# Performance work log

Measured on AMD Instinct MI355X. Metric: run time of the kernel, lower is better.

Reference implementation:

```python
import jax, jax.numpy as jnp
import numpy as np

N = 50000   # total nodes across batched graphs
E = 800000  # total edges
F = 30      # input node features
G = 256     # number of graphs in the disjoint batch
CH = [128, 64, 32]
N_LABELS = 2


def setup_inputs() -> dict:
    key = jax.random.key(0)
    ks = jax.random.split(key, 16)
    x = jax.random.normal(ks[0], (N, F), dtype=jnp.float32)
    edge_weight = jax.random.uniform(ks[1], (E,), dtype=jnp.float32)
    edge_row = jax.random.randint(ks[2], (E,), 0, N, dtype=jnp.int32)
    edge_col = jax.random.randint(ks[3], (E,), 0, N, dtype=jnp.int32)
    seg = jnp.sort(jax.random.randint(ks[4], (N,), 0, G, dtype=jnp.int32))
    # GCSConv params: out = A @ (x W1) + x W2 + b, per layer
    dims = [F] + CH
    params = {}
    kk = 5
    for l in range(3):
        fin, fout = dims[l], dims[l + 1]
        s = 1.0 / np.sqrt(fin)
        params[f"w1_{l+1}"] = jax.random.uniform(ks[kk], (fin, fout), minval=-s, maxval=s, dtype=jnp.float32); kk += 1
        params[f"w2_{l+1}"] = jax.random.uniform(ks[kk], (fin, fout), minval=-s, maxval=s, dtype=jnp.float32); kk += 1
        params[f"b_{l+1}"] = jnp.zeros((fout,), dtype=jnp.float32)
    sd = 1.0 / np.sqrt(CH[-1])
    params["wd"] = jax.random.uniform(ks[kk], (CH[-1], N_LABELS), minval=-sd, maxval=sd, dtype=jnp.float32)
    params["bd"] = jnp.zeros((N_LABELS,), dtype=jnp.float32)
    return {"x": x, "edge_weight": edge_weight, "edge_row": edge_row,
            "edge_col": edge_col, "seg": seg, **params}


def _gcs_conv(x, ew, er, ec, w1, w2, b):
    # spektral GCSConv: relu(A @ (x W1) + x W2 + b) with sparse A in COO form
    h = x @ w1                                   # [N, Fout]
    msgs = ew[:, None] * h[ec]                   # gather along edges [E, Fout]
    agg = jax.ops.segment_sum(msgs, er, num_segments=N)  # SpMM scatter [N, Fout]
    return jax.nn.relu(agg + x @ w2 + b)


def reference(x, edge_weight, edge_row, edge_col, seg,
              w1_1, w2_1, b_1, w1_2, w2_2, b_2, w1_3, w2_3, b_3, wd, bd):
    h = _gcs_conv(x, edge_weight, edge_row, edge_col, w1_1, w2_1, b_1)
    h = _gcs_conv(h, edge_weight, edge_row, edge_col, w1_2, w2_2, b_2)
    h = _gcs_conv(h, edge_weight, edge_row, edge_col, w1_3, w2_3, b_3)
    # GlobalAvgPool: segment mean over graph ids
    sums = jax.ops.segment_sum(h, seg, num_segments=G)               # [G, 32]
    cnts = jax.ops.segment_sum(jnp.ones((N,), h.dtype), seg, num_segments=G)
    pooled = sums / jnp.maximum(cnts, 1.0)[:, None]
    return jax.nn.softmax(pooled @ wd + bd, axis=-1)                 # [G, 2]
```

## Files before the change

kernel.cpp:

```cpp
#include <hip/hip_runtime.h>
#include <hip/hip_fp16.h>

#define N_NODES 50000
#define N_EDGES 800000
#define N_GRAPHS 256
#define NCB 196
#define CHUNK 3125
#define MBLK 782

typedef _Float16 f16x8 __attribute__((ext_vector_type(8)));
typedef float    f32x4 __attribute__((ext_vector_type(4)));

__global__ __launch_bounds__(256)
void hist_prep(const int* __restrict__ ER, const float* __restrict__ X,
               const int* __restrict__ SEG,
               const float* __restrict__ W1, const float* __restrict__ W2,
               const float* __restrict__ W12, const float* __restrict__ W22,
               const float* __restrict__ W13, const float* __restrict__ W23,
               int* __restrict__ ghist, __half* __restrict__ XPh,
               int* __restrict__ start,
               __half* __restrict__ W1f, __half* __restrict__ W2f,
               __half* __restrict__ W3f)
{
    int b = blockIdx.x;
    int t = threadIdx.x;
    if (b < 256) {
        __shared__ int h[NCB];
        for (int i = t; i < NCB; i += 256) h[i] = 0;
        __syncthreads();
        int lo = b * CHUNK, hi = lo + CHUNK;
        for (int e = lo + t; e < hi; e += 256) atomicAdd(&h[ER[e] >> 8], 1);
        __syncthreads();
        for (int i = t; i < NCB; i += 256) ghist[i * 256 + b] = h[i];
        return;
    }
    int bid = b - 256;
    if (bid < 782) {
        int idx = bid * 256 + t;
        int n = idx >> 2;
        int c4 = idx & 3;
        if (n >= N_NODES) return;
        __half2 hb[4];
        #pragma unroll
        for (int k = 0; k < 4; ++k) {
            int c0 = c4 * 8 + 2 * k;
            float v0 = (c0 < 30) ? X[n * 30 + c0] : 0.f;
            float v1 = (c0 + 1 < 30) ? X[n * 30 + c0 + 1] : 0.f;
            hb[k] = __float22half2_rn(make_float2(v0, v1));
        }
        *(uint4*)(XPh + (size_t)n * 32 + c4 * 8) = *(uint4*)&hb[0];
    } else if (bid < 978) {
        int n = (bid - 782) * 256 + t;
        if (n >= N_NODES) return;
        int g = SEG[n];
        int gprev = (n == 0) ? -1 : SEG[n - 1];
        for (int gg = gprev + 1; gg <= g; ++gg) start[gg] = n;
        if (n == N_NODES - 1)
            for (int gg = g + 1; gg <= N_GRAPHS; ++gg) start[gg] = N_NODES;
    } else {
        int idx = (bid - 978) * 256 + t;
        if (idx < 8192) {
            int i = idx & 7, c = (idx >> 3) & 15, g = (idx >> 7) & 3;
            int s = (idx >> 9) & 1, n = idx >> 10;
            int k = s * 32 + g * 8 + i, col = n * 16 + c;
            float w = 0.f;
            if (k < 30) w = W1[k * 128 + col];
            else if (k >= 32 && k < 62) w = W2[(k - 32) * 128 + col];
            W1f[idx] = __float2half(w);
        } else if (idx < 24576) {
            int o = idx - 8192;
            int i = o & 7, c = (o >> 3) & 15, g = (o >> 7) & 3;
            int s = (o >> 9) & 3, n = o >> 11;
            int k = s * 32 + g * 8 + i, col = n * 16 + c;
            float w = (col < 64) ? W12[k * 64 + col] : W22[k * 64 + col - 64];
            W2f[o] = __float2half(w);
        } else {
            int o = idx - 24576;
            int i = o & 7, c = (o >> 3) & 15, g = (o >> 7) & 3;
            int s = (o >> 9) & 1, n = o >> 10;
            int k = s * 32 + g * 8 + i, col = n * 16 + c;
            float w = (col < 32) ? W13[k * 32 + col] : W23[k * 32 + col - 32];
            W3f[o] = __float2half(w);
        }
    }
}

__global__ __launch_bounds__(256)
void scan1(int* __restrict__ ghist, int* __restrict__ bsum)
{
    __shared__ int s[256];
    int t = threadIdx.x, b = blockIdx.x;
    int i = b * 256 + t;
    int v = ghist[i];
    s[t] = v;
    __syncthreads();
    for (int off = 1; off < 256; off <<= 1) {
        int u = (t >= off) ? s[t - off] : 0;
        __syncthreads();
        s[t] += u;
        __syncthreads();
    }
    ghist[i] = s[t] - v;
    if (t == 255) bsum[b] = s[255];
}

__global__ __launch_bounds__(256)
void c_scatter(const int* __restrict__ ER, const int* __restrict__ EC,
               const float* __restrict__ EW, const int* __restrict__ ghist,
               const int* __restrict__ bsum, uint2* __restrict__ tmp)
{
    __shared__ int s[256];
    __shared__ int cur[NCB];
    int t = threadIdx.x, blk = blockIdx.x;
    int v = (t < NCB) ? bsum[t] : 0;
    s[t] = v;
    __syncthreads();
    for (int off = 1; off < 256; off <<= 1) {
        int u = (t >= off) ? s[t - off] : 0;
        __syncthreads();
        s[t] += u;
        __syncthreads();
    }
    if (t < NCB) cur[t] = (s[t] - v) + ghist[t * 256 + blk];
    __syncthreads();
    int lo = blk * CHUNK, hi = lo + CHUNK;
    for (int e = lo + t; e < hi; e += 256) {
        int d = ER[e];
        int pos = atomicAdd(&cur[d >> 8], 1);
        tmp[pos] = make_uint2((unsigned int)EC[e] | ((unsigned int)(d & 255) << 16),
                              (unsigned int)__half_as_ushort(__float2half(EW[e])));
    }
}

__device__ __forceinline__ void fma8h(float4& a0, float4& a1, float w,
                                      const uint4& raw)
{
    const __half2* hp = (const __half2*)&raw;
    float2 f0 = __half22float2(hp[0]);
    float2 f1 = __half22float2(hp[1]);
    float2 f2 = __half22float2(hp[2]);
    float2 f3 = __half22float2(hp[3]);
    a0.x = fmaf(w, f0.x, a0.x); a0.y = fmaf(w, f0.y, a0.y);
    a0.z = fmaf(w, f1.x, a0.z); a0.w = fmaf(w, f1.y, a0.w);
    a1.x = fmaf(w, f2.x, a1.x); a1.y = fmaf(w, f2.y, a1.y);
    a1.z = fmaf(w, f3.x, a1.z); a1.w = fmaf(w, f3.y, a1.w);
}

__device__ __forceinline__ unsigned int relu2(unsigned int u)
{
    unsigned int lo = (u & 0x8000u)     ? 0u : (u & 0x0000FFFFu);
    unsigned int hi = (u & 0x80000000u) ? 0u : (u & 0xFFFF0000u);
    return lo | hi;
}

__global__ __launch_bounds__(1024)
void bsort(const uint2* __restrict__ tmp, const int* __restrict__ bsum,
           unsigned int* __restrict__ packed, int* __restrict__ rowptr)
{
    __shared__ int s[256];
    __shared__ int hist[256];
    __shared__ int cur[256];
    int t = threadIdx.x, b = blockIdx.x;

    if (t < 256) s[t] = (t < NCB) ? bsum[t] : 0;
    __syncthreads();
    for (int off = 1; off < 256; off <<= 1) {
        int u = 0;
        if (t < 256 && t >= off) u = s[t - off];
        __syncthreads();
        if (t < 256) s[t] += u;
        __syncthreads();
    }
    int cntb = bsum[b];
    int base = s[b] - cntb;
    int end  = base + cntb;
    __syncthreads();

    if (t < 256) hist[t] = 0;
    __syncthreads();
    for (int j = base + t; j < end; j += 1024)
        atomicAdd(&hist[(tmp[j].x >> 16) & 255], 1);
    __syncthreads();
    int hv = 0;
    if (t < 256) { hv = hist[t]; s[t] = hv; }
    __syncthreads();
    for (int off = 1; off < 256; off <<= 1) {
        int u = 0;
        if (t < 256 && t >= off) u = s[t - off];
        __syncthreads();
        if (t < 256) s[t] += u;
        __syncthreads();
    }
    if (t < 256) {
        int excl = s[t] - hv;
        int n = b * 256 + t;
        if (n < N_NODES) rowptr[n] = base + excl;
        if (b == NCB - 1 && t == 0) rowptr[N_NODES] = N_EDGES;
        cur[t] = base + excl;
    }
    __syncthreads();
    for (int j = base + t; j < end; j += 1024) {
        uint2 v = tmp[j];
        int pos = atomicAdd(&cur[(v.x >> 16) & 255], 1);
        packed[pos] = (v.x & 0xFFFF) | (v.y << 16);
    }
}

__global__ __launch_bounds__(512)
void dense12_mfma(const __half* __restrict__ XPh, const int* __restrict__ rowptr,
                  const unsigned int* __restrict__ packed,
                  const __half* __restrict__ W1f, const float* __restrict__ B1,
                  const __half* __restrict__ W2f, const float* __restrict__ B2,
                  __half* __restrict__ H2h, __half* __restrict__ A2h)
{
    __shared__ __align__(16) __half As[64 * 72];
    __shared__ __align__(16) __half Hs[64 * 136];
    const int tid = threadIdx.x;
    const int m0 = blockIdx.x * 64;

    if (tid < 256) {
        int row = tid >> 2, c4 = tid & 3;
        int gm = m0 + row;
        uint4 v = make_uint4(0, 0, 0, 0);
        if (gm < N_NODES) v = *(const uint4*)(XPh + (size_t)gm * 32 + c4 * 8);
        *(uint4*)(As + row * 72 + (4 + c4) * 8) = v;
    }
    {
        int local = tid >> 3;
        int es = (tid >> 2) & 1;
        int q = tid & 3;
        int n = m0 + local;
        float4 acc0 = make_float4(0.f, 0.f, 0.f, 0.f);
        float4 acc1 = make_float4(0.f, 0.f, 0.f, 0.f);
        if (n < N_NODES) {
            int r0 = rowptr[n], r1 = rowptr[n + 1];
            int mid = (r0 + r1) >> 1;
            int lo = es ? mid : r0;
            int hi = es ? r1 : mid;
            int j = lo;
            for (; j + 3 < hi; j += 4) {
                unsigned int ra = packed[j],     rb = packed[j + 1];
                unsigned int rc = packed[j + 2], rd = packed[j + 3];
                uint4 rawa = *(const uint4*)(XPh + (size_t)(ra & 0xFFFF) * 32 + q * 8);
                uint4 rawb = *(const uint4*)(XPh + (size_t)(rb & 0xFFFF) * 32 + q * 8);
                uint4 rawc = *(const uint4*)(XPh + (size_t)(rc & 0xFFFF) * 32 + q * 8);
                uint4 rawd = *(const uint4*)(XPh + (size_t)(rd & 0xFFFF) * 32 + q * 8);
                float wa = __half2float(__ushort_as_half((unsigned short)(ra >> 16)));
                float wb = __half2float(__ushort_as_half((unsigned short)(rb >> 16)));
                float wc = __half2float(__ushort_as_half((unsigned short)(rc >> 16)));
                float wd = __half2float(__ushort_as_half((unsigned short)(rd >> 16)));
                fma8h(acc0, acc1, wa, rawa);
                fma8h(acc0, acc1, wb, rawb);
                fma8h(acc0, acc1, wc, rawc);
                fma8h(acc0, acc1, wd, rawd);
            }
            for (; j < hi; ++j) {
                unsigned int r = packed[j];
                uint4 raw = *(const uint4*)(XPh + (size_t)(r & 0xFFFF) * 32 + q * 8);
                float wv = __half2float(__ushort_as_half((unsigned short)(r >> 16)));
                fma8h(acc0, acc1, wv, raw);
            }
        }
        float* part = (float*)Hs;
        if (es == 1) {
            *(float4*)&part[local * 36 + q * 8 + 0] = acc0;
            *(float4*)&part[local * 36 + q * 8 + 4] = acc1;
        }
        __syncthreads();
        if (es == 0) {
            float4 p0 = *(float4*)&part[local * 36 + q * 8 + 0];
            float4 p1 = *(float4*)&part[local * 36 + q * 8 + 4];
            acc0.x += p0.x; acc0.y += p0.y; acc0.z += p0.z; acc0.w += p0.w;
            acc1.x += p1.x; acc1.y += p1.y; acc1.z += p1.z; acc1.w += p1.w;
            __half2 hb2[4];
            hb2[0] = __float22half2_rn(make_float2(acc0.x, acc0.y));
            hb2[1] = __float22half2_rn(make_float2(acc0.z, acc0.w));
            hb2[2] = __float22half2_rn(make_float2(acc1.x, acc1.y));
            hb2[3] = __float22half2_rn(make_float2(acc1.z, acc1.w));
            *(uint4*)(As + local * 72 + q * 8) = *(uint4*)&hb2[0];
        }
    }
    __syncthreads();

    const int lane = tid & 63;
    const int w  = tid >> 6;
    const int lr = lane & 15;
    const int lg = lane >> 4;

    f32x4 acc[4];
    #pragma unroll
    for (int m = 0; m < 4; ++m) acc[m] = (f32x4){0.f, 0.f, 0.f, 0.f};

    #pragma unroll
    for (int s = 0; s < 2; ++s) {
        f16x8 b = *(const f16x8*)(W1f + (((w * 2 + s) * 4 + lg) * 16 + lr) * 8);
        #pragma unroll
        for (int m = 0; m < 4; ++m) {
            f16x8 a = *(const f16x8*)(As + (m * 16 + lr) * 72 + s * 32 + lg * 8);
            acc[m] = __builtin_amdgcn_mfma_f32_16x16x32_f16(a, b, acc[m], 0, 0, 0);
        }
    }

    {
        const float bias = B1[w * 16 + lr];
        #pragma unroll
        for (int m = 0; m < 4; ++m)
            #pragma unroll
            for (int r = 0; r < 4; ++r) {
                float v = fmaxf(acc[m][r] + bias, 0.f);
                Hs[(m * 16 + lg * 4 + r) * 136 + w * 16 + lr] = __float2half(v);
            }
    }
    __syncthreads();

    f32x4 acc2[4];
    #pragma unroll
    for (int m = 0; m < 4; ++m) acc2[m] = (f32x4){0.f, 0.f, 0.f, 0.f};

    #pragma unroll
    for (int s = 0; s < 4; ++s) {
        f16x8 b = *(const f16x8*)(W2f + (((w * 4 + s) * 4 + lg) * 16 + lr) * 8);
        #pragma unroll
        for (int m = 0; m < 4; ++m) {
            f16x8 a = *(const f16x8*)(Hs + (m * 16 + lr) * 136 + s * 32 + lg * 8);
            acc2[m] = __builtin_amdgcn_mfma_f32_16x16x32_f16(a, b, acc2[m], 0, 0, 0);
        }
    }
    __syncthreads();

    {
        const float bias = (w >= 4) ? B2[(w - 4) * 16 + lr] : 0.f;
        #pragma unroll
        for (int m = 0; m < 4; ++m)
            #pragma unroll
            for (int r = 0; r < 4; ++r)
                Hs[(m * 16 + lg * 4 + r) * 136 + w * 16 + lr] =
                    __float2half(acc2[m][r] + bias);
    }
    __syncthreads();

    for (int idx = tid; idx < 1024; idx += 512) {
        int row = idx >> 4, c8 = idx & 15;
        int gm = m0 + row;
        if (gm < N_NODES) {
            uint4 v = *(const uint4*)(Hs + row * 136 + c8 * 8);
            if (c8 < 8) *(uint4*)(H2h + (size_t)gm * 64 + c8 * 8) = v;
            else        *(uint4*)(A2h + (size_t)gm * 64 + (c8 - 8) * 8) = v;
        }
    }
}

__global__ __launch_bounds__(256)
void dense3_mfma(const __half* __restrict__ X, const __half* __restrict__ W3f,
                 const float* __restrict__ B3, __half* __restrict__ H3h,
                 __half* __restrict__ B2h)
{
    __shared__ __align__(16) __half As[64 * 72];
    __shared__ __align__(16) __half Os[64 * 72];
    const int tid = threadIdx.x;
    const int m0 = blockIdx.x * 64;
    const int lane = tid & 63;
    const int w  = tid >> 6;
    const int lr = lane & 15;
    const int lg = lane >> 4;

    for (int idx = tid; idx < 512; idx += 256) {
        int row = idx >> 3, c8 = idx & 7;
        int gm = m0 + row;
        uint4 v = make_uint4(0, 0, 0, 0);
        if (gm < N_NODES) v = *(const uint4*)(X + (size_t)gm * 64 + c8 * 8);
        v.x = relu2(v.x); v.y = relu2(v.y); v.z = relu2(v.z); v.w = relu2(v.w);
        *(uint4*)(As + row * 72 + c8 * 8) = v;
    }
    __syncthreads();

    f32x4 acc[4];
    #pragma unroll
    for (int m = 0; m < 4; ++m) acc[m] = (f32x4){0.f, 0.f, 0.f, 0.f};

    #pragma unroll
    for (int s = 0; s < 2; ++s) {
        f16x8 b = *(const f16x8*)(W3f + (((w * 2 + s) * 4 + lg) * 16 + lr) * 8);
        #pragma unroll
        for (int m = 0; m < 4; ++m) {
            f16x8 a = *(const f16x8*)(As + (m * 16 + lr) * 72 + s * 32 + lg * 8);
            acc[m] = __builtin_amdgcn_mfma_f32_16x16x32_f16(a, b, acc[m], 0, 0, 0);
        }
    }

    const float bias = (w >= 2) ? B3[(w - 2) * 16 + lr] : 0.f;
    #pragma unroll
    for (int m = 0; m < 4; ++m)
        #pragma unroll
        for (int r = 0; r < 4; ++r)
            Os[(m * 16 + lg * 4 + r) * 72 + w * 16 + lr] =
                __float2half(acc[m][r] + bias);
    __syncthreads();

    for (int idx = tid; idx < 512; idx += 256) {
        int row = idx >> 3, c8 = idx & 7;
        int gm = m0 + row;
        if (gm < N_NODES) {
            uint4 v = *(const uint4*)(Os + row * 72 + c8 * 8);
            if (c8 < 4) *(uint4*)(H3h + (size_t)gm * 32 + c8 * 8) = v;
            else        *(uint4*)(B2h + (size_t)gm * 32 + (c8 - 4) * 8) = v;
        }
    }
}

template<int FOUT, int S>
__global__ __launch_bounds__(512)
void spmm_split(const __half* __restrict__ H, const int* __restrict__ rowptr,
                const unsigned int* __restrict__ packed, __half* __restrict__ AGGh)
{
    constexpr int T = FOUT / 8;
    constexpr int NPB = 512 / (S * T);
    __shared__ float part[NPB][S - 1][FOUT + 4];
    int tid = threadIdx.x;
    int local = tid / (S * T);
    int rem = tid % (S * T);
    int s = rem / T;
    int q = rem % T;
    int n = blockIdx.x * NPB + local;
    bool valid = (n < N_NODES);
    float4 acc0 = make_float4(0.f, 0.f, 0.f, 0.f);
    float4 acc1 = make_float4(0.f, 0.f, 0.f, 0.f);
    __half* ap = AGGh + (size_t)n * FOUT + q * 8;
    if (valid) {
        int r0 = rowptr[n], r1 = rowptr[n + 1];
        int deg = r1 - r0;
        int lo = r0 + (deg * s) / S;
        int hi = r0 + (deg * (s + 1)) / S;
        if (s == 0) {
            uint4 raw = *(const uint4*)ap;
            const __half2* hp = (const __half2*)&raw;
            float2 f0 = __half22float2(hp[0]);
            float2 f1 = __half22float2(hp[1]);
            float2 f2 = __half22float2(hp[2]);
            float2 f3 = __half22float2(hp[3]);
            acc0 = make_float4(f0.x, f0.y, f1.x, f1.y);
            acc1 = make_float4(f2.x, f2.y, f3.x, f3.y);
        }
        int j = lo;
        for (; j + 3 < hi; j += 4) {
            unsigned int ra = packed[j],     rb = packed[j + 1];
            unsigned int rc = packed[j + 2], rd = packed[j + 3];
            uint4 rawa = *(const uint4*)(H + (size_t)(ra & 0xFFFF) * FOUT + q * 8);
            uint4 rawb = *(const uint4*)(H + (size_t)(rb & 0xFFFF) * FOUT + q * 8);
            uint4 rawc = *(const uint4*)(H + (size_t)(rc & 0xFFFF) * FOUT + q * 8);
            uint4 rawd = *(const uint4*)(H + (size_t)(rd & 0xFFFF) * FOUT + q * 8);
            float wa = __half2float(__ushort_as_half((unsigned short)(ra >> 16)));
            float wb = __half2float(__ushort_as_half((unsigned short)(rb >> 16)));
            float wc = __half2float(__ushort_as_half((unsigned short)(rc >> 16)));
            float wd = __half2float(__ushort_as_half((unsigned short)(rd >> 16)));
            fma8h(acc0, acc1, wa, rawa);
            fma8h(acc0, acc1, wb, rawb);
            fma8h(acc0, acc1, wc, rawc);
            fma8h(acc0, acc1, wd, rawd);
        }
        for (; j < hi; ++j) {
            unsigned int r = packed[j];
            uint4 raw = *(const uint4*)(H + (size_t)(r & 0xFFFF) * FOUT + q * 8);
            float w = __half2float(__ushort_as_half((unsigned short)(r >> 16)));
            fma8h(acc0, acc1, w, raw);
        }
    }
    if (s > 0) {
        *(float4*)&part[local][s - 1][q * 8 + 0] = acc0;
        *(float4*)&part[local][s - 1][q * 8 + 4] = acc1;
    }
    __syncthreads();
    if (s == 0 && valid) {
        #pragma unroll
        for (int ss = 0; ss < S - 1; ++ss) {
            float4 p0 = *(float4*)&part[local][ss][q * 8 + 0];
            float4 p1 = *(float4*)&part[local][ss][q * 8 + 4];
            acc0.x += p0.x; acc0.y += p0.y; acc0.z += p0.z; acc0.w += p0.w;
            acc1.x += p1.x; acc1.y += p1.y; acc1.z += p1.z; acc1.w += p1.w;
        }
        __half2 hb[4];
        hb[0] = __float22half2_rn(make_float2(acc0.x, acc0.y));
        hb[1] = __float22half2_rn(make_float2(acc0.z, acc0.w));
        hb[2] = __float22half2_rn(make_float2(acc1.x, acc1.y));
        hb[3] = __float22half2_rn(make_float2(acc1.z, acc1.w));
        *(uint4*)ap = *(uint4*)&hb[0];
    }
}

__global__ __launch_bounds__(1024)
void pool_kernel(const __half* __restrict__ H, const int* __restrict__ start,
                 const float* __restrict__ WD, const float* __restrict__ BD,
                 float* __restrict__ OUT)
{
    __shared__ float red[32][33];
    int g = blockIdx.x;
    int s = start[g], e = start[g + 1];
    int q = threadIdx.x & 31;
    int grp = threadIdx.x >> 5;
    float acc = 0.f;
    for (int n = s + grp; n < e; n += 32)
        acc += fmaxf(__half2float(H[(size_t)n * 32 + q]), 0.f);
    red[grp][q] = acc;
    __syncthreads();
    if (threadIdx.x < 32) {
        float v = 0.f;
        #pragma unroll
        for (int i = 0; i < 32; ++i) v += red[i][q];
        float inv = (e > s) ? 1.0f / (float)(e - s) : 1.0f;
        float p = v * inv;
        float p0 = p * WD[q * 2 + 0];
        float p1 = p * WD[q * 2 + 1];
        #pragma unroll
        for (int off = 16; off; off >>= 1) {
            p0 += __shfl_down(p0, off, 32);
            p1 += __shfl_down(p1, off, 32);
        }
        if (q == 0) {
            float l0 = p0 + BD[0], l1 = p1 + BD[1];
            float m = fmaxf(l0, l1);
            float e0 = expf(l0 - m), e1 = expf(l1 - m);
            float si = 1.0f / (e0 + e1);
            OUT[g * 2 + 0] = e0 * si;
            OUT[g * 2 + 1] = e1 * si;
        }
    }
}

extern "C" void kernel_launch(void* const* d_in, const int* in_sizes, int n_in,
                              void* d_out, int out_size, void* d_ws, size_t ws_size,
                              hipStream_t stream)
{
    const float* x    = (const float*)d_in[0];
    const float* ew   = (const float*)d_in[1];
    const int*   er   = (const int*)d_in[2];
    const int*   ec   = (const int*)d_in[3];
    const int*   seg  = (const int*)d_in[4];
    const float* w1_1 = (const float*)d_in[5];
    const float* w2_1 = (const float*)d_in[6];
    const float* b_1  = (const float*)d_in[7];
    const float* w1_2 = (const float*)d_in[8];
    const float* w2_2 = (const float*)d_in[9];
    const float* b_2  = (const float*)d_in[10];
    const float* w1_3 = (const float*)d_in[11];
    const float* w2_3 = (const float*)d_in[12];
    const float* b_3  = (const float*)d_in[13];
    const float* wd   = (const float*)d_in[14];
    const float* bd   = (const float*)d_in[15];

    float* ws = (float*)d_ws;
    int*   IW = (int*)d_ws;
    __half* XPh    = (__half*)ws;
    uint2*  tmp    = (uint2*)(ws + 1600000);
    __half* H2h    = (__half*)(ws + 3200000);
    __half* A2h    = (__half*)(ws + 4800000);
    __half* H3h    = (__half*)(ws + 6400000);
    __half* B2h    = (__half*)(ws + 7200000);
    unsigned int* packed = (unsigned int*)(IW + 8000000);
    int*    rowptr = IW + 9000000;
    int*    ghist  = IW + 9060000;
    int*    bsum   = IW + 9115000;
    int*    start  = IW + 9120000;
    __half* W1f    = (__half*)(ws + 9125000);
    __half* W2f    = (__half*)(ws + 9130000);
    __half* W3f    = (__half*)(ws + 9139000);

    dim3 blk(256);

    hist_prep<<<dim3(256 + 782 + 196 + 112), blk, 0, stream>>>(
        er, x, seg, w1_1, w2_1, w1_2, w2_2, w1_3, w2_3,
        ghist, XPh, start, W1f, W2f, W3f);
    scan1<<<dim3(NCB), blk, 0, stream>>>(ghist, bsum);
    c_scatter<<<dim3(256), blk, 0, stream>>>(er, ec, ew, ghist, bsum, tmp);
    bsort<<<dim3(NCB), dim3(1024), 0, stream>>>(tmp, bsum, packed, rowptr);

    dense12_mfma<<<dim3(MBLK), dim3(512), 0, stream>>>(XPh, rowptr, packed,
                                                       W1f, b_1, W2f, b_2,
                                                       H2h, A2h);
    spmm_split<64, 4><<<dim3((N_NODES + 15) / 16), dim3(512), 0, stream>>>(H2h, rowptr,
                                                                           packed, A2h);
    dense3_mfma<<<dim3(MBLK), blk, 0, stream>>>(A2h, W3f, b_3, H3h, B2h);
    spmm_split<32, 4><<<dim3((N_NODES + 31) / 32), dim3(512), 0, stream>>>(H3h, rowptr,
                                                                           packed, B2h);

    pool_kernel<<<dim3(N_GRAPHS), dim3(1024), 0, stream>>>(B2h, start, wd, bd,
                                                           (float*)d_out);
}
```

Before: 172.8 us.

## Fuse layer-2 SpMM aggregation with layer-3 dense MFMA into one kernel

Replaces the separate spmm_split<64,4> launch and dense3_mfma launch with a single 1024-thread kernel. Each block first aggregates the neighbour rows for its 64 nodes into shared memory, splitting each node's edges across two thread groups, then adds the self term, applies ReLU and runs the 16x16x32 MFMA for layer 3. This removes one launch and the global round trip of the layer-2 aggregate. In exchange, each block has only two edge splits per node instead of four, and the MFMA work is spread so each wave handles a single tile.

```diff
diff --git a/kernel.cpp b/kernel.cpp
--- a/kernel.cpp
+++ b/kernel.cpp
@@ -144,13 +144,6 @@
     a0.z = fmaf(w, f1.x, a0.z); a0.w = fmaf(w, f1.y, a0.w);
     a1.x = fmaf(w, f2.x, a1.x); a1.y = fmaf(w, f2.y, a1.y);
     a1.z = fmaf(w, f3.x, a1.z); a1.w = fmaf(w, f3.y, a1.w);
-}
-
-__device__ __forceinline__ unsigned int relu2(unsigned int u)
-{
-    unsigned int lo = (u & 0x8000u)     ? 0u : (u & 0x0000FFFFu);
-    unsigned int hi = (u & 0x80000000u) ? 0u : (u & 0xFFFF0000u);
-    return lo | hi;
 }
 
 __global__ __launch_bounds__(1024)
@@ -350,55 +343,108 @@
     }
 }
 
-__global__ __launch_bounds__(256)
-void dense3_mfma(const __half* __restrict__ X, const __half* __restrict__ W3f,
+__global__ __launch_bounds__(1024)
+void spmm_dense3(const __half* __restrict__ H2h, const int* __restrict__ rowptr,
+                 const unsigned int* __restrict__ packed,
+                 const __half* __restrict__ A2h, const __half* __restrict__ W3f,
                  const float* __restrict__ B3, __half* __restrict__ H3h,
                  __half* __restrict__ B2h)
 {
     __shared__ __align__(16) __half As[64 * 72];
     __shared__ __align__(16) __half Os[64 * 72];
+    __shared__ float part[64][68];
     const int tid = threadIdx.x;
     const int m0 = blockIdx.x * 64;
+
+    {
+        int local = tid >> 4;
+        int es = (tid >> 3) & 1;
+        int q = tid & 7;
+        int n = m0 + local;
+        float4 acc0 = make_float4(0.f, 0.f, 0.f, 0.f);
+        float4 acc1 = make_float4(0.f, 0.f, 0.f, 0.f);
+        if (n < N_NODES) {
+            int r0 = rowptr[n], r1 = rowptr[n + 1];
+            int mid = (r0 + r1) >> 1;
+            int lo = es ? mid : r0;
+            int hi = es ? r1 : mid;
+            if (es == 0) {
+                uint4 raw = *(const uint4*)(A2h + (size_t)n * 64 + q * 8);
+                const __half2* hp = (const __half2*)&raw;
+                float2 f0 = __half22float2(hp[0]);
+                float2 f1 = __half22float2(hp[1]);
+                float2 f2 = __half22float2(hp[2]);
+                float2 f3 = __half22float2(hp[3]);
+                acc0 = make_float4(f0.x, f0.y, f1.x, f1.y);
+                acc1 = make_float4(f2.x, f2.y, f3.x, f3.y);
+            }
+            int j = lo;
+            for (; j + 3 < hi; j += 4) {
+                unsigned int ra = packed[j],     rb = packed[j + 1];
+                unsigned int rc = packed[j + 2], rd = packed[j + 3];
+                uint4 rawa = *(const uint4*)(H2h + (size_t)(ra & 0xFFFF) * 64 + q * 8);
+                uint4 rawb = *(const uint4*)(H2h + (size_t)(rb & 0xFFFF) * 64 + q * 8);
+                uint4 rawc = *(const uint4*)(H2h + (size_t)(rc & 0xFFFF) * 64 + q * 8);
+                uint4 rawd = *(const uint4*)(H2h + (size_t)(rd & 0xFFFF) * 64 + q * 8);
+                float wa = __half2float(__ushort_as_half((unsigned short)(ra >> 16)));
+                float wb = __half2float(__ushort_as_half((unsigned short)(rb >> 16)));
+                float wc = __half2float(__ushort_as_half((unsigned short)(rc >> 16)));
+                float wd = __half2float(__ushort_as_half((unsigned short)(rd >> 16)));
+                fma8h(acc0, acc1, wa, rawa);
+                fma8h(acc0, acc1, wb, rawb);
+                fma8h(acc0, acc1, wc, rawc);
+                fma8h(acc0, acc1, wd, rawd);
+            }
+            for (; j < hi; ++j) {
+                unsigned int r = packed[j];
+                uint4 raw = *(const uint4*)(H2h + (size_t)(r & 0xFFFF) * 64 + q * 8);
+                float w = __half2float(__ushort_as_half((unsigned short)(r >> 16)));
+                fma8h(acc0, acc1, w, raw);
+            }
+        }
+        if (es == 1) {
+            *(float4*)&part[local][q * 8 + 0] = acc0;
+            *(float4*)&part[local][q * 8 + 4] = acc1;
+        }
+        __syncthreads();
+        if (es == 0) {
+            float4 p0 = *(float4*)&part[local][q * 8 + 0];
+            float4 p1 = *(float4*)&part[local][q * 8 + 4];
+            acc0.x += p0.x; acc0.y += p0.y; acc0.z += p0.z; acc0.w += p0.w;
+            acc1.x += p1.x; acc1.y += p1.y; acc1.z += p1.z; acc1.w += p1.w;
+            __half2 hb[4];
+            hb[0] = __float22half2_rn(make_float2(fmaxf(acc0.x, 0.f), fmaxf(acc0.y, 0.f)));
+            hb[1] = __float22half2_rn(make_float2(fmaxf(acc0.z, 0.f), fmaxf(acc0.w, 0.f)));
+            hb[2] = __float22half2_rn(make_float2(fmaxf(acc1.x, 0.f), fmaxf(acc1.y, 0.f)));
+            hb[3] = __float22half2_rn(make_float2(fmaxf(acc1.z, 0.f), fmaxf(acc1.w, 0.f)));
+            *(uint4*)(As + local * 72 + q * 8) = *(uint4*)&hb[0];
+        }
+    }
+    __syncthreads();
+
     const int lane = tid & 63;
     const int w  = tid >> 6;
+    const int wm = w >> 2;
+    const int wn = w & 3;
     const int lr = lane & 15;
     const int lg = lane >> 4;
 
-    for (int idx = tid; idx < 512; idx += 256) {
-        int row = idx >> 3, c8 = idx & 7;
-        int gm = m0 + row;
-        uint4 v = make_uint4(0, 0, 0, 0);
-        if (gm < N_NODES) v = *(const uint4*)(X + (size_t)gm * 64 + c8 * 8);
-        v.x = relu2(v.x); v.y = relu2(v.y); v.z = relu2(v.z); v.w = relu2(v.w);
-        *(uint4*)(As + row * 72 + c8 * 8) = v;
-    }
-    __syncthreads();
-
-    f32x4 acc[4];
-    #pragma unroll
-    for (int m = 0; m < 4; ++m) acc[m] = (f32x4){0.f, 0.f, 0.f, 0.f};
-
+    f32x4 acc = (f32x4){0.f, 0.f, 0.f, 0.f};
     #pragma unroll
     for (int s = 0; s < 2; ++s) {
-        f16x8 b = *(const f16x8*)(W3f + (((w * 2 + s) * 4 + lg) * 16 + lr) * 8);
-        #pragma unroll
-        for (int m = 0; m < 4; ++m) {
-            f16x8 a = *(const f16x8*)(As + (m * 16 + lr) * 72 + s * 32 + lg * 8);
-            acc[m] = __builtin_amdgcn_mfma_f32_16x16x32_f16(a, b, acc[m], 0, 0, 0);
-        }
-    }
-
-    const float bias = (w >= 2) ? B3[(w - 2) * 16 + lr] : 0.f;
+        f16x8 b = *(const f16x8*)(W3f + (((wn * 2 + s) * 4 + lg) * 16 + lr) * 8);
+        f16x8 a = *(const f16x8*)(As + (wm * 16 + lr) * 72 + s * 32 + lg * 8);
+        acc = __builtin_amdgcn_mfma_f32_16x16x32_f16(a, b, acc, 0, 0, 0);
+    }
+
+    const float bias = (wn >= 2) ? B3[(wn - 2) * 16 + lr] : 0.f;
     #pragma unroll
-    for (int m = 0; m < 4; ++m)
-        #pragma unroll
-        for (int r = 0; r < 4; ++r)
-            Os[(m * 16 + lg * 4 + r) * 72 + w * 16 + lr] =
-                __float2half(acc[m][r] + bias);
-    __syncthreads();
-
-    for (int idx = tid; idx < 512; idx += 256) {
-        int row = idx >> 3, c8 = idx & 7;
+    for (int r = 0; r < 4; ++r)
+        Os[(wm * 16 + lg * 4 + r) * 72 + wn * 16 + lr] = __float2half(acc[r] + bias);
+    __syncthreads();
+
+    if (tid < 512) {
+        int row = tid >> 3, c8 = tid & 7;
         int gm = m0 + row;
         if (gm < N_NODES) {
             uint4 v = *(const uint4*)(Os + row * 72 + c8 * 8);
@@ -576,9 +622,8 @@
     dense12_mfma<<<dim3(MBLK), dim3(512), 0, stream>>>(XPh, rowptr, packed,
                                                        W1f, b_1, W2f, b_2,
                                                        H2h, A2h);
-    spmm_split<64, 4><<<dim3((N_NODES + 15) / 16), dim3(512), 0, stream>>>(H2h, rowptr,
-                                                                           packed, A2h);
-    dense3_mfma<<<dim3(MBLK), blk, 0, stream>>>(A2h, W3f, b_3, H3h, B2h);
+    spmm_dense3<<<dim3(MBLK), dim3(1024), 0, stream>>>(H2h, rowptr, packed, A2h,
+                                                       W3f, b_3, H3h, B2h);
     spmm_split<32, 4><<<dim3((N_NODES + 31) / 32), dim3(512), 0, stream>>>(H3h, rowptr,
                                                                            packed, B2h);
 
```

New measurement: 166.6 us. 3.6% less time.
